# Kernel optimization log

Measured on AMD Instinct MI355X. Metric: run time of the kernel, lower is better.

## Reference

```python
import jax, jax.numpy as jnp
import numpy as np

B = 1024          # batch of subject-object pairs
D_IN_HALF = 2048  # sbj/obj feature width; cat -> input_len = 4096
D_OUT = 1024      # output_len (embedding / label-vec width)
N_LABELS = 128    # number of relation labels in codebook


def setup_inputs() -> dict:
    key = jax.random.key(0)
    ks = jax.random.split(key, 7)
    s = 0.02  # small init scale for weights
    return {
        "sbj_vec": jax.random.normal(ks[0], (B, D_IN_HALF), jnp.float32),
        "obj_vec": jax.random.normal(ks[1], (B, D_IN_HALF), jnp.float32),
        "W1": jax.random.normal(ks[2], (2 * D_IN_HALF, D_OUT), jnp.float32) * s,
        "b1": jax.random.normal(ks[3], (D_OUT,), jnp.float32) * s,
        "W2": jax.random.normal(ks[4], (D_OUT, D_OUT), jnp.float32) * s,
        "b2": jax.random.normal(ks[5], (D_OUT,), jnp.float32) * s,
        "label_vecs": jax.random.normal(ks[6], (N_LABELS, D_OUT), jnp.float32),
    }


def reference(sbj_vec, obj_vec, W1, b1, W2, b2, label_vecs):
    # Sequential(ReLU, Dropout(eval=identity), Linear) applied twice.
    x = jnp.concatenate([sbj_vec, obj_vec], axis=1)          # [B, 2*D_IN_HALF]
    hidden = jax.nn.relu(x) @ W1 + b1                        # [B, D_OUT]
    emb = jax.nn.relu(hidden) @ W2 + b2                      # [B, D_OUT]
    # order_sim vs every label vector, fully batched (replaces per-sample loop):
    # sim[b, l] = -|| relu(label_vecs[l] - emb[b]) ||_2
    diff = jax.nn.relu(label_vecs[None, :, :] - emb[:, None, :])  # [B, L, D_OUT]
    scores = -jnp.sqrt(jnp.sum(diff * diff, axis=2))              # [B, L]
    return scores
```

## Files before the change

### kernel.cpp

```cpp
#include <hip/hip_runtime.h>
#include <math.h>

constexpr int Bn = 1024, DH = 2048, K1 = 4096, DO = 1024, NL = 128;
constexpr int MN = Bn * DO;

typedef __bf16 bf16x8 __attribute__((ext_vector_type(8)));
typedef short  s16x8  __attribute__((ext_vector_type(8)));
typedef float  f32x4  __attribute__((ext_vector_type(4)));

__device__ __forceinline__ unsigned short f2bf(float f) {
  union { float f; unsigned u; } v; v.f = f;
  unsigned r = v.u + 0x7FFFu + ((v.u >> 16) & 1u);
  return (unsigned short)(r >> 16);
}

__global__ __launch_bounds__(256)
void prep(const float* __restrict__ sbj, const float* __restrict__ obj,
          const float* __restrict__ W1, const float* __restrict__ W2,
          unsigned short* __restrict__ Abf,
          unsigned short* __restrict__ W1t, unsigned short* __restrict__ W2t) {
  const int tid = threadIdx.x;
  if (blockIdx.x < 2048) {
    const int t = blockIdx.x * 256 + tid;
    const int m = t >> 9;
    const int k = (t & 511) << 3;
    const float* src = (k < DH) ? sbj + (size_t)m * DH + k
                                : obj + (size_t)m * DH + (k - DH);
    const float4 a = ((const float4*)src)[0];
    const float4 b = ((const float4*)src)[1];
    uint4 o;
    o.x = (unsigned)f2bf(fmaxf(a.x, 0.f)) | ((unsigned)f2bf(fmaxf(a.y, 0.f)) << 16);
    o.y = (unsigned)f2bf(fmaxf(a.z, 0.f)) | ((unsigned)f2bf(fmaxf(a.w, 0.f)) << 16);
    o.z = (unsigned)f2bf(fmaxf(b.x, 0.f)) | ((unsigned)f2bf(fmaxf(b.y, 0.f)) << 16);
    o.w = (unsigned)f2bf(fmaxf(b.z, 0.f)) | ((unsigned)f2bf(fmaxf(b.w, 0.f)) << 16);
    *(uint4*)&Abf[(size_t)m * K1 + k] = o;
    return;
  }
  __shared__ float tl[64][65];
  const int tb = blockIdx.x - 2048;
  int by = tb >> 4;
  const int c0 = (tb & 15) * 64;
  const float* in; unsigned short* out; int R;
  if (by < 64) { in = W1; out = W1t; R = K1; }
  else         { in = W2; out = W2t; R = DO; by -= 64; }
  const int r0 = by * 64;
  {
    const int rr = tid >> 4, cc = (tid & 15) * 4;
    #pragma unroll
    for (int i = 0; i < 4; ++i) {
      const float4 v = *(const float4*)&in[(size_t)(r0 + rr + i * 16) * DO + c0 + cc];
      tl[rr + i * 16][cc + 0] = v.x; tl[rr + i * 16][cc + 1] = v.y;
      tl[rr + i * 16][cc + 2] = v.z; tl[rr + i * 16][cc + 3] = v.w;
    }
  }
  __syncthreads();
  {
    const int r4 = (tid & 15) * 4;
    #pragma unroll
    for (int i = 0; i < 4; ++i) {
      const int cr = i * 16 + (tid >> 4);
      uint2 o;
      o.x = (unsigned)f2bf(tl[r4 + 0][cr]) | ((unsigned)f2bf(tl[r4 + 1][cr]) << 16);
      o.y = (unsigned)f2bf(tl[r4 + 2][cr]) | ((unsigned)f2bf(tl[r4 + 3][cr]) << 16);
      *(uint2*)&out[(size_t)(c0 + cr) * R + r0 + r4] = o;
    }
  }
}

template <int KSLICE>
__global__ __launch_bounds__(256, 4)
void mfma_gemm(const unsigned short* __restrict__ A,
               const unsigned short* __restrict__ Bt,
               float* __restrict__ P, int K) {
  __shared__ __align__(16) unsigned short smem[2 * 64 * 128];
  unsigned short* LA = smem;
  unsigned short* LB = smem + 64 * 128;

  const int tid = threadIdx.x;
  const int w = tid >> 6, l = tid & 63;
  const int m0 = blockIdx.y * 64, n0 = blockIdx.x * 64;
  const int kb = blockIdx.z * KSLICE;

  f32x4 acc[4][4] = {};

  constexpr int NIT = KSLICE / 128;
  for (int it = 0; it < NIT; ++it) {
    const int k0 = kb + it * 128;
    #pragma unroll
    for (int i = 0; i < 4; ++i) {
      const int c = i * 256 + tid, m = c >> 4, kc = c & 15;
      const int kcg = (kc & 8) | ((kc & 7) ^ (m & 7));
      __builtin_amdgcn_global_load_lds(
          (const __attribute__((address_space(1))) unsigned int*)(A + (size_t)(m0 + m) * K + k0 + kcg * 8),
          (__attribute__((address_space(3))) unsigned int*)&LA[c * 8], 16, 0, 0);
    }
    #pragma unroll
    for (int i = 0; i < 4; ++i) {
      const int c = i * 256 + tid, n = c >> 4, kc = c & 15;
      const int kcg = (kc & 8) | ((kc & 7) ^ (n & 7));
      __builtin_amdgcn_global_load_lds(
          (const __attribute__((address_space(1))) unsigned int*)(Bt + (size_t)(n0 + n) * K + k0 + kcg * 8),
          (__attribute__((address_space(3))) unsigned int*)&LB[c * 8], 16, 0, 0);
    }
    __syncthreads();

    const int kcq = w * 4 + (l >> 4);
    bf16x8 af[4], bfr[4];
    #pragma unroll
    for (int i = 0; i < 4; ++i) {
      const int r = i * 16 + (l & 15);
      const int kca = (kcq & 8) | ((kcq & 7) ^ (r & 7));
      af[i]  = __builtin_bit_cast(bf16x8, *(const s16x8*)&LA[(r * 16 + kca) * 8]);
      bfr[i] = __builtin_bit_cast(bf16x8, *(const s16x8*)&LB[(r * 16 + kca) * 8]);
    }
    #pragma unroll
    for (int i = 0; i < 4; ++i)
      #pragma unroll
      for (int j = 0; j < 4; ++j)
        acc[i][j] = __builtin_amdgcn_mfma_f32_16x16x32_bf16(af[i], bfr[j], acc[i][j], 0, 0, 0);
    __syncthreads();
  }

  float* red = (float*)smem;
  auto writeacc = [&](float* dst) {
    #pragma unroll
    for (int i = 0; i < 4; ++i)
      #pragma unroll
      for (int j = 0; j < 4; ++j)
        *(f32x4*)&dst[((i * 4 + j) * 64 + l) * 4] = acc[i][j];
  };
  auto addacc = [&](const float* src) {
    #pragma unroll
    for (int i = 0; i < 4; ++i)
      #pragma unroll
      for (int j = 0; j < 4; ++j)
        acc[i][j] += *(const f32x4*)&src[((i * 4 + j) * 64 + l) * 4];
  };
  if (w >= 2) writeacc(red + (w - 2) * 4096);
  __syncthreads();
  if (w < 2) addacc(red + w * 4096);
  __syncthreads();
  if (w == 1) writeacc(red);
  __syncthreads();
  if (w != 0) return;
  addacc(red);

  float* Pz = P + (size_t)blockIdx.z * MN;
  #pragma unroll
  for (int i = 0; i < 4; ++i) {
    #pragma unroll
    for (int r = 0; r < 4; ++r) {
      const int m = m0 + i * 16 + (l >> 4) * 4 + r;
      #pragma unroll
      for (int j = 0; j < 4; ++j) {
        const int n = n0 + j * 16 + (l & 15);
        Pz[(size_t)m * DO + n] = acc[i][j][r];
      }
    }
  }
}

template <int KS, bool RELU, bool OUT_BF16>
__global__ __launch_bounds__(256)
void combine(const float* __restrict__ P, const float* __restrict__ bias,
             void* __restrict__ out) {
  const int row = blockIdx.x, t = threadIdx.x;
  const size_t i4 = (size_t)row * 256 + t;
  f32x4 s = ((const f32x4*)P)[i4];
  #pragma unroll
  for (int c = 1; c < KS; ++c) s += ((const f32x4*)P)[(size_t)c * (MN / 4) + i4];
  const f32x4 bb = *(const f32x4*)&bias[t * 4];
  s += bb;
  if (RELU) {
    s[0] = fmaxf(s[0], 0.f); s[1] = fmaxf(s[1], 0.f);
    s[2] = fmaxf(s[2], 0.f); s[3] = fmaxf(s[3], 0.f);
  }
  if (OUT_BF16) {
    uint2 o;
    o.x = (unsigned)f2bf(s[0]) | ((unsigned)f2bf(s[1]) << 16);
    o.y = (unsigned)f2bf(s[2]) | ((unsigned)f2bf(s[3]) << 16);
    *(uint2*)((unsigned short*)out + (size_t)row * DO + t * 4) = o;
  } else {
    *(f32x4*)((float*)out + (size_t)row * DO + t * 4) = s;
  }
}

__global__ __launch_bounds__(256)
void score_partial(const float* __restrict__ emb, const float* __restrict__ labels,
                   float* __restrict__ SP) {
  __shared__ float es[64][33];
  __shared__ float ls[64][132];
  const int tid = threadIdx.x;
  const int b0 = blockIdx.x * 32;
  const int d0 = blockIdx.y * 64;

  #pragma unroll
  for (int i = 0; i < 2; ++i) {
    const int fi = tid + i * 256;
    const int b = fi >> 4, dq = fi & 15;
    const float4 v = *(const float4*)&emb[(size_t)(b0 + b) * DO + d0 + dq * 4];
    es[dq * 4 + 0][b] = v.x; es[dq * 4 + 1][b] = v.y;
    es[dq * 4 + 2][b] = v.z; es[dq * 4 + 3][b] = v.w;
  }
  #pragma unroll
  for (int i = 0; i < 8; ++i) {
    const int fi = tid + i * 256;
    const int lr = fi >> 4, dq = fi & 15;
    const float4 v = *(const float4*)&labels[(size_t)lr * DO + d0 + dq * 4];
    ls[dq * 4 + 0][lr] = v.x; ls[dq * 4 + 1][lr] = v.y;
    ls[dq * 4 + 2][lr] = v.z; ls[dq * 4 + 3][lr] = v.w;
  }
  __syncthreads();

  const int tb = tid & 15;
  const int tl = tid >> 4;
  float acc[2][8] = {};

  for (int dd = 0; dd < 64; ++dd) {
    const float e0 = es[dd][tb * 2 + 0];
    const float e1 = es[dd][tb * 2 + 1];
    const float4 l0 = *(const float4*)&ls[dd][tl * 8];
    const float4 l1 = *(const float4*)&ls[dd][tl * 8 + 4];
    const float lv[8] = {l0.x, l0.y, l0.z, l0.w, l1.x, l1.y, l1.z, l1.w};
    #pragma unroll
    for (int j = 0; j < 8; ++j) {
      float t0 = fmaxf(lv[j] - e0, 0.f); acc[0][j] = fmaf(t0, t0, acc[0][j]);
      float t1 = fmaxf(lv[j] - e1, 0.f); acc[1][j] = fmaf(t1, t1, acc[1][j]);
    }
  }

  float* SPz = SP + (size_t)blockIdx.y * (Bn * NL);
  #pragma unroll
  for (int i = 0; i < 2; ++i) {
    const size_t base = (size_t)(b0 + tb * 2 + i) * NL + tl * 8;
    float4 v0 = {acc[i][0], acc[i][1], acc[i][2], acc[i][3]};
    float4 v1 = {acc[i][4], acc[i][5], acc[i][6], acc[i][7]};
    *(float4*)&SPz[base]     = v0;
    *(float4*)&SPz[base + 4] = v1;
  }
}

__global__ __launch_bounds__(256)
void score_reduce(const float* __restrict__ SP, float* __restrict__ out) {
  const size_t i4 = (size_t)blockIdx.x * 256 + threadIdx.x;
  f32x4 s = ((const f32x4*)SP)[i4];
  #pragma unroll
  for (int c = 1; c < 16; ++c) s += ((const f32x4*)SP)[(size_t)c * 32768 + i4];
  f32x4 o = {-sqrtf(s[0]), -sqrtf(s[1]), -sqrtf(s[2]), -sqrtf(s[3])};
  ((f32x4*)out)[i4] = o;
}

extern "C" void kernel_launch(void* const* d_in, const int* in_sizes, int n_in,
                              void* d_out, int out_size, void* d_ws, size_t ws_size,
                              hipStream_t stream) {
  const float* sbj  = (const float*)d_in[0];
  const float* obj  = (const float*)d_in[1];
  const float* W1   = (const float*)d_in[2];
  const float* b1   = (const float*)d_in[3];
  const float* W2   = (const float*)d_in[4];
  const float* b2   = (const float*)d_in[5];
  const float* labs = (const float*)d_in[6];
  float* scores = (float*)d_out;

  char* ws = (char*)d_ws;
  unsigned short* Abf = (unsigned short*)(ws);
  unsigned short* W1t = (unsigned short*)(ws + (8ull << 20));
  unsigned short* W2t = (unsigned short*)(ws + (16ull << 20));
  unsigned short* H   = (unsigned short*)(ws + (18ull << 20));
  float* P  = (float*)(ws + (24ull << 20));
  float* E  = (float*)(ws + (40ull << 20));
  float* SP = (float*)(ws + (44ull << 20));

  dim3 blk(256);
  prep<<<dim3(2048 + 1280), blk, 0, stream>>>(sbj, obj, W1, W2, Abf, W1t, W2t);

  mfma_gemm<1024><<<dim3(16, 16, 4), blk, 0, stream>>>(Abf, W1t, P, K1);
  combine<4, true, true><<<dim3(Bn), blk, 0, stream>>>(P, b1, H);
  mfma_gemm<256><<<dim3(16, 16, 4), blk, 0, stream>>>(H, W2t, P, DO);
  combine<4, false, false><<<dim3(Bn), blk, 0, stream>>>(P, b2, E);

  score_partial<<<dim3(32, 16), blk, 0, stream>>>(E, labs, SP);
  score_reduce<<<dim3(128), blk, 0, stream>>>(SP, scores);
}
```

Measured before the change: 146.4 us.

## Swizzle GEMM block order, split epilogue across two waves, fuse second combine into scoring

The GEMM grid is flattened to 1D and remapped so that groups of eight consecutive blocks cover a 4x8 tile patch within the same K slice, aiming for better L2 reuse across XCDs. The final reduction now has two waves each writing half of the output tile instead of one wave writing all of it. The second split-K combine kernel is removed and its summation plus bias add are folded into score_partial's load of the embedding, which drops one launch and one round trip of the fp32 embedding buffer. In exchange score_partial reads four partial buffers, and those reads repeat across the blocks that share rows.

```diff
diff --git a/kernel.cpp b/kernel.cpp
--- a/kernel.cpp
+++ b/kernel.cpp
@@ -78,8 +78,14 @@
 
   const int tid = threadIdx.x;
   const int w = tid >> 6, l = tid & 63;
-  const int m0 = blockIdx.y * 64, n0 = blockIdx.x * 64;
-  const int kb = blockIdx.z * KSLICE;
+
+  const int bid = blockIdx.x;
+  const int g = bid & 7, t = bid >> 3;
+  const int x = (g & 3) * 4 + (t & 3);
+  const int y = (g >> 2) * 8 + ((t >> 2) & 7);
+  const int z = t >> 5;
+  const int m0 = y * 64, n0 = x * 64;
+  const int kb = z * KSLICE;
 
   f32x4 acc[4][4] = {};
 
@@ -122,32 +128,31 @@
   }
 
   float* red = (float*)smem;
-  auto writeacc = [&](float* dst) {
-    #pragma unroll
-    for (int i = 0; i < 4; ++i)
+  auto writeacc = [&](float* dst, int ilo, int ihi) {
+    for (int i = ilo; i < ihi; ++i)
       #pragma unroll
       for (int j = 0; j < 4; ++j)
         *(f32x4*)&dst[((i * 4 + j) * 64 + l) * 4] = acc[i][j];
   };
-  auto addacc = [&](const float* src) {
-    #pragma unroll
-    for (int i = 0; i < 4; ++i)
+  auto addacc = [&](const float* src, int ilo, int ihi) {
+    for (int i = ilo; i < ihi; ++i)
       #pragma unroll
       for (int j = 0; j < 4; ++j)
         acc[i][j] += *(const f32x4*)&src[((i * 4 + j) * 64 + l) * 4];
   };
-  if (w >= 2) writeacc(red + (w - 2) * 4096);
-  __syncthreads();
-  if (w < 2) addacc(red + w * 4096);
-  __syncthreads();
-  if (w == 1) writeacc(red);
-  __syncthreads();
-  if (w != 0) return;
-  addacc(red);
-
-  float* Pz = P + (size_t)blockIdx.z * MN;
-  #pragma unroll
-  for (int i = 0; i < 4; ++i) {
+  if (w >= 2) writeacc(red + (w - 2) * 4096, 0, 4);
+  __syncthreads();
+  if (w < 2) addacc(red + w * 4096, 0, 4);
+  __syncthreads();
+  if (w == 1) writeacc(red, 0, 2);
+  if (w == 0) writeacc(red, 2, 4);
+  __syncthreads();
+  if (w >= 2) return;
+  const int ilo = (w == 0) ? 0 : 2;
+  addacc(red, ilo, ilo + 2);
+
+  float* Pz = P + (size_t)z * MN;
+  for (int i = ilo; i < ilo + 2; ++i) {
     #pragma unroll
     for (int r = 0; r < 4; ++r) {
       const int m = m0 + i * 16 + (l >> 4) * 4 + r;
@@ -186,8 +191,8 @@
 }
 
 __global__ __launch_bounds__(256)
-void score_partial(const float* __restrict__ emb, const float* __restrict__ labels,
-                   float* __restrict__ SP) {
+void score_partial(const float* __restrict__ P, const float* __restrict__ b2,
+                   const float* __restrict__ labels, float* __restrict__ SP) {
   __shared__ float es[64][33];
   __shared__ float ls[64][132];
   const int tid = threadIdx.x;
@@ -198,9 +203,13 @@
   for (int i = 0; i < 2; ++i) {
     const int fi = tid + i * 256;
     const int b = fi >> 4, dq = fi & 15;
-    const float4 v = *(const float4*)&emb[(size_t)(b0 + b) * DO + d0 + dq * 4];
-    es[dq * 4 + 0][b] = v.x; es[dq * 4 + 1][b] = v.y;
-    es[dq * 4 + 2][b] = v.z; es[dq * 4 + 3][b] = v.w;
+    const size_t idx = ((size_t)(b0 + b) * DO + d0 + dq * 4) / 4;
+    f32x4 v = ((const f32x4*)P)[idx];
+    #pragma unroll
+    for (int c = 1; c < 4; ++c) v += ((const f32x4*)P)[(size_t)c * (MN / 4) + idx];
+    v += *(const f32x4*)&b2[d0 + dq * 4];
+    es[dq * 4 + 0][b] = v[0]; es[dq * 4 + 1][b] = v[1];
+    es[dq * 4 + 2][b] = v[2]; es[dq * 4 + 3][b] = v[3];
   }
   #pragma unroll
   for (int i = 0; i < 8; ++i) {
@@ -268,17 +277,14 @@
   unsigned short* W2t = (unsigned short*)(ws + (16ull << 20));
   unsigned short* H   = (unsigned short*)(ws + (18ull << 20));
   float* P  = (float*)(ws + (24ull << 20));
-  float* E  = (float*)(ws + (40ull << 20));
-  float* SP = (float*)(ws + (44ull << 20));
+  float* SP = (float*)(ws + (40ull << 20));
 
   dim3 blk(256);
   prep<<<dim3(2048 + 1280), blk, 0, stream>>>(sbj, obj, W1, W2, Abf, W1t, W2t);
 
-  mfma_gemm<1024><<<dim3(16, 16, 4), blk, 0, stream>>>(Abf, W1t, P, K1);
+  mfma_gemm<1024><<<dim3(1024), blk, 0, stream>>>(Abf, W1t, P, K1);
   combine<4, true, true><<<dim3(Bn), blk, 0, stream>>>(P, b1, H);
-  mfma_gemm<256><<<dim3(16, 16, 4), blk, 0, stream>>>(H, W2t, P, DO);
-  combine<4, false, false><<<dim3(Bn), blk, 0, stream>>>(P, b2, E);
-
-  score_partial<<<dim3(32, 16), blk, 0, stream>>>(E, labs, SP);
+  mfma_gemm<256><<<dim3(1024), blk, 0, stream>>>(H, W2t, P, DO);
+  score_partial<<<dim3(32, 16), blk, 0, stream>>>(P, b2, labs, SP);
   score_reduce<<<dim3(128), blk, 0, stream>>>(SP, scores);
 }
```

Result: slower. 335.1 us (+128.8%).
